# Kernel tuning notes

Measured on AMD Instinct MI355X. Metric: run time of the kernel, lower is better.

## Reference

```python
import jax, jax.numpy as jnp
import numpy as np

VX, VY = 0.2, 0.2
X_OFF = VX / 2 + 0.0          # vx/2 + pc_range[0]
Y_OFF = VY / 2 + (-40.0)      # vy/2 + pc_range[1]
K = 8                          # hardcoded in GCNLayer
BN_EPS = 1e-3
LRELU_SLOPE = 0.2
V, T, C_IN, C_OUT = 4096, 100, 4, 64


def _gcn_layer(x, conv_w, bn_gamma, bn_beta, bn_mean, bn_var):
    """DGCNN EdgeConv layer. x: [N, T, C]. Returns [N, T, O]."""
    N, Tn, C = x.shape
    # KNN on negative squared distance (self included in topk, as in torch code)
    xx = jnp.sum(x * x, axis=-1)                       # [N, T]
    inner = jnp.einsum('ntc,nsc->nts', x, x)           # [N, T, T]
    neg_dist = 2.0 * inner - xx[:, :, None] - xx[:, None, :]
    _, idx = jax.lax.top_k(neg_dist, K)                # [N, T, K]
    # gather neighbor features: nbr[n,t,k,c] = x[n, idx[n,t,k], c]
    nbr = x[jnp.arange(N)[:, None, None], idx]         # [N, T, K, C]
    xc = x[:, :, None, :]                              # [N, T, 1, C]
    edge = jnp.concatenate(
        [nbr - xc, jnp.broadcast_to(xc, (N, Tn, K, C))], axis=-1)  # [N,T,K,2C]
    # 1x1 conv (no bias) + eval-mode BatchNorm + LeakyReLU(0.2)
    h = jnp.einsum('ntkc,oc->ntko', edge, conv_w)      # [N, T, K, O]
    scale = bn_gamma / jnp.sqrt(bn_var + BN_EPS)
    h = (h - bn_mean) * scale + bn_beta
    h = jax.nn.leaky_relu(h, LRELU_SLOPE)
    return jnp.max(h, axis=2)                          # max over k -> [N, T, O]


def setup_inputs() -> dict:
    key = jax.random.key(0)
    k1, k2, k3, k4, k5, k6 = jax.random.split(key, 6)
    features = jax.random.normal(k1, (V, T, C_IN), dtype=jnp.float32)
    num_voxels = jnp.maximum(
        jax.random.randint(k2, (V,), 0, T), 1).astype(jnp.int32)
    coors = jax.random.randint(k3, (V, 4), 0, 352).astype(jnp.int32)
    # GCNLayer params: Conv2d(18, 64, 1, bias=False) + BatchNorm2d(64)
    conv_w = jax.random.normal(k4, (C_OUT, 18), dtype=jnp.float32) * 0.1
    bn_gamma = jnp.ones((C_OUT,), jnp.float32)
    bn_beta = jnp.zeros((C_OUT,), jnp.float32)
    bn_mean = jax.random.normal(k5, (C_OUT,), jnp.float32) * 0.1
    bn_var = 1.0 + 0.1 * jax.random.uniform(k6, (C_OUT,), jnp.float32)
    return {"features": features, "conv_w": conv_w, "bn_gamma": bn_gamma,
            "bn_beta": bn_beta, "bn_mean": bn_mean, "bn_var": bn_var,
            "num_voxels": num_voxels, "coors": coors}


def reference(features, conv_w, bn_gamma, bn_beta, bn_mean, bn_var,
              num_voxels, coors):
    nv = num_voxels.astype(features.dtype)
    # decorate: cluster offsets (xyz - mean) and pillar-center offsets (xy)
    points_mean = jnp.sum(features[:, :, :3], axis=1, keepdims=True) / nv[:, None, None]
    f_cluster = features[:, :, :3] - points_mean                      # [V,T,3]
    fx = features[:, :, 0] - (coors[:, 3].astype(features.dtype)[:, None] * VX + X_OFF)
    fy = features[:, :, 1] - (coors[:, 2].astype(features.dtype)[:, None] * VY + Y_OFF)
    f_center = jnp.stack([fx, fy], axis=-1)                           # [V,T,2]
    feat = jnp.concatenate([features, f_cluster, f_center], axis=-1)  # [V,T,9]
    # padding mask: point t valid iff t < num_voxels[v]
    mask = (jnp.arange(T)[None, :] < num_voxels[:, None]).astype(features.dtype)
    feat = feat * mask[:, :, None]
    # single GCN (last) layer; batch_process chunking is a no-op mathematically
    out = _gcn_layer(feat, conv_w, bn_gamma, bn_beta, bn_mean, bn_var)  # [V,T,64]
    out = out * mask[:, :, None]            # (+ zeros prev_features_out)
    out = jnp.max(out, axis=1)              # max over points -> [V, 64]
    return out
```

## Files before the change

### kernel.cpp

```cpp
#include <hip/hip_runtime.h>

#define TPTS 100
#define CO   64
#define KK   8

__device__ __forceinline__ unsigned umin_(unsigned a, unsigned b) { return a < b ? a : b; }
__device__ __forceinline__ unsigned umax_(unsigned a, unsigned b) { return a > b ? a : b; }

__device__ __forceinline__ unsigned med3u(unsigned a, unsigned b, unsigned c) {
    unsigned d;
    asm("v_med3_u32 %0, %1, %2, %3" : "=v"(d) : "v"(a), "v"(b), "v"(c));
    return d;
}

__device__ __forceinline__ unsigned dist_key(const float4 qt, const float4 qs, unsigned s) {
    float dx = qt.x - qs.x, dy = qt.y - qs.y;
    float dz = qt.z - qs.z, dw = qt.w - qs.w;
    float e = __fmaf_rn(dx, dx, __fmaf_rn(dy, dy, __fmaf_rn(dz, dz, dw * dw)));
    return (__float_as_uint(e) & 0xFFFFFF80u) | s;
}

__device__ __forceinline__ void ins8(unsigned val[KK], unsigned key) {
    #pragma unroll
    for (int k = KK - 1; k >= 1; --k)
        val[k] = med3u(val[k - 1], val[k], key);
    val[0] = umin_(val[0], key);
}

__global__ __launch_bounds__(256) void dgcnn_kernel(
    const float* __restrict__ features,
    const float* __restrict__ conv_w,
    const float* __restrict__ bn_gamma,
    const float* __restrict__ bn_beta,
    const float* __restrict__ bn_mean,
    const float* __restrict__ bn_var,
    const int*  __restrict__ num_voxels,
    const int*  __restrict__ coors,
    float* __restrict__ out)
{
    __shared__ float    s_feat[TPTS][12];
    __shared__ float    s_xx[TPTS];
    __shared__ unsigned s_idxp[TPTS][2];
    __shared__ float    s_red[4][CO];
    __shared__ float    s_mean[4];
    __shared__ union {
        float    stage[TPTS][4];
        _Float16 g16[TPTS][CO];
    } s_u;

    const float INF = __builtin_inff();
    const int v   = blockIdx.x;
    const int tid = threadIdx.x;
    const int nv  = num_voxels[v];

    float4 f = make_float4(0.f, 0.f, 0.f, 0.f);
    if (tid < TPTS) {
        f = reinterpret_cast<const float4*>(features)[v * TPTS + tid];
        *reinterpret_cast<float4*>(&s_u.stage[tid][0]) = f;
    }
    __syncthreads();

    if (tid < 96) {
        int ch = tid >> 5, j = tid & 31;
        float p = s_u.stage[j][ch] + s_u.stage[j + 32][ch] + s_u.stage[j + 64][ch];
        if (j < 4) p += s_u.stage[j + 96][ch];
        #pragma unroll
        for (int off = 16; off >= 1; off >>= 1)
            p += __shfl_xor(p, off, 32);
        if (j == 0) s_mean[ch] = p / (float)nv;
    }
    __syncthreads();

    if (tid < TPTS) {
        float mask = (tid < nv) ? 1.0f : 0.0f;
        float c3 = (float)coors[v * 4 + 3];
        float c2 = (float)coors[v * 4 + 2];
        float r0 = f.x * mask, r1 = f.y * mask, r2 = f.z * mask, r3 = f.w * mask;
        float r4 = (f.x - s_mean[0]) * mask;
        float r5 = (f.y - s_mean[1]) * mask;
        float r6 = (f.z - s_mean[2]) * mask;
        float r7 = (f.x - (c3 * 0.2f + 0.1f)) * mask;
        float r8 = (f.y - (c2 * 0.2f - 39.9f)) * mask;
        float xx = r0*r0 + r1*r1 + r2*r2 + r3*r3 + r4*r4
                 + r5*r5 + r6*r6 + r7*r7 + r8*r8;
        float4* rowv = reinterpret_cast<float4*>(&s_feat[tid][0]);
        rowv[0] = make_float4(1.7320508075688772f * r0,
                              1.7320508075688772f * r1,
                              1.4142135623730951f * r2, r3);
        rowv[1] = make_float4(r4, r5, r6, r7);
        rowv[2] = make_float4(r8, 0.f, 0.f, 0.f);
        s_xx[tid] = xx;
    }

    const int o  = tid & 63;
    const int wv = tid >> 6;
    const float sgn = (bn_gamma[o] < 0.f) ? -1.f : 1.f;
    float w1[9], w2[9];
    #pragma unroll
    for (int c = 0; c < 9; ++c) {
        const float ws = (c == 0 || c == 1) ? 0.57735026918962576f
                       : (c == 2) ? 0.70710678118654752f : 1.f;
        float a = conv_w[o * 18 + c];
        float b = conv_w[o * 18 + 9 + c];
        w1[c] = a * sgn * ws;
        w2[c] = (b - a) * sgn * ws;
    }
    __syncthreads();

    const int nd = (nv + 31) >> 5;

    if (wv < nd) {
        const int trow = wv * 32 + (o & 31);
        const int bsd  = o >> 5;
        if (trow < nv) {
            const float4 qt = *reinterpret_cast<const float4*>(&s_feat[trow][0]);
            unsigned val[KK];
            #pragma unroll
            for (int k = 0; k < KK; ++k) val[k] = 0xFFFFFFFFu;
            int mcnt = TPTS - nv; if (mcnt > KK) mcnt = KK;
            int ha = (nv + mcnt + 1) >> 1; if (ha > nv) ha = nv;
            int s        = bsd ? ha : 0;
            const int se = bsd ? nv : ha;
            #pragma unroll 2
            for (; s < se; ++s) {
                const float4 qs = *reinterpret_cast<const float4*>(&s_feat[s][0]);
                ins8(val, dist_key(qt, qs, (unsigned)s));
            }
            if (bsd) {
                unsigned kmb = __float_as_uint(s_xx[trow]) & 0xFFFFFF80u;
                for (int j = 0; j < mcnt; ++j)
                    ins8(val, kmb | (unsigned)(nv + j));
            }
            unsigned other[KK];
            #pragma unroll
            for (int k = 0; k < KK; ++k) other[k] = __shfl_xor(val[k], 32);
            if (!bsd) {
                unsigned m[KK];
                #pragma unroll
                for (int k = 0; k < KK; ++k)
                    m[k] = umin_(val[k], other[KK - 1 - k]) & 127u;
                unsigned p0 = m[0] | (m[1] << 8) | (m[2] << 16) | (m[3] << 24);
                unsigned p1 = m[4] | (m[5] << 8) | (m[6] << 16) | (m[7] << 24);
                *reinterpret_cast<uint2*>(&s_idxp[trow][0]) = make_uint2(p0, p1);
            }
        }
    }

    {
        int r0 = nv + wv, r1 = nv + wv + 4;
        if (r0 < TPTS) s_u.g16[r0][o] = (_Float16)0.f;
        if (r1 < TPTS) s_u.g16[r1][o] = (_Float16)0.f;
    }

    {
        int sR, step;
        if (nd <= 2) { sR = (wv >= nd) ? (wv - nd) : nv; step = 4 - nd; }
        else         { sR = wv;                          step = 4;      }
        for (; sR < nv; sR += step) {
            const float4* row = reinterpret_cast<const float4*>(&s_feat[sR][0]);
            float4 a = row[0], b = row[1];
            float c8 = s_feat[sR][8];
            float g = a.x * w1[0];
            g = __fmaf_rn(a.y, w1[1], g);
            g = __fmaf_rn(a.z, w1[2], g);
            g = __fmaf_rn(a.w, w1[3], g);
            g = __fmaf_rn(b.x, w1[4], g);
            g = __fmaf_rn(b.y, w1[5], g);
            g = __fmaf_rn(b.z, w1[6], g);
            g = __fmaf_rn(b.w, w1[7], g);
            g = __fmaf_rn(c8,  w1[8], g);
            s_u.g16[sR][o] = (_Float16)g;
        }
    }
    __syncthreads();

    float acc = -INF;
    for (int tt = wv; tt < nv; tt += 4) {
        const float4* row = reinterpret_cast<const float4*>(&s_feat[tt][0]);
        float4 a = row[0], b = row[1];
        float c8 = s_feat[tt][8];
        float base = a.x * w2[0];
        base = __fmaf_rn(a.y, w2[1], base);
        base = __fmaf_rn(a.z, w2[2], base);
        base = __fmaf_rn(a.w, w2[3], base);
        base = __fmaf_rn(b.x, w2[4], base);
        base = __fmaf_rn(b.y, w2[5], base);
        base = __fmaf_rn(b.z, w2[6], base);
        base = __fmaf_rn(b.w, w2[7], base);
        base = __fmaf_rn(c8,  w2[8], base);
        uint2 pk = *reinterpret_cast<const uint2*>(&s_idxp[tt][0]);
        int i0 =  pk.x        & 255, i1 = (pk.x >>  8) & 255;
        int i2 = (pk.x >> 16) & 255, i3 = (pk.x >> 24) & 255;
        int i4 =  pk.y        & 255, i5 = (pk.y >>  8) & 255;
        int i6 = (pk.y >> 16) & 255, i7 = (pk.y >> 24) & 255;
        float g0 = (float)s_u.g16[i0][o], g1 = (float)s_u.g16[i1][o];
        float g2 = (float)s_u.g16[i2][o], g3 = (float)s_u.g16[i3][o];
        float g4 = (float)s_u.g16[i4][o], g5 = (float)s_u.g16[i5][o];
        float g6 = (float)s_u.g16[i6][o], g7 = (float)s_u.g16[i7][o];
        float gm = fmaxf(fmaxf(fmaxf(g0, g1), fmaxf(g2, g3)),
                         fmaxf(fmaxf(g4, g5), fmaxf(g6, g7)));
        acc = fmaxf(acc, gm + base);
    }
    s_red[wv][o] = acc;
    __syncthreads();

    if (tid < CO) {
        float m = fmaxf(fmaxf(s_red[0][tid], s_red[1][tid]),
                        fmaxf(s_red[2][tid], s_red[3][tid]));
        float scale = bn_gamma[tid] / sqrtf(bn_var[tid] + 0.001f);
        float bias  = bn_beta[tid] - bn_mean[tid] * scale;
        float h = m * fabsf(scale) + bias;
        float a = (h > 0.f) ? h : 0.2f * h;
        if (nv < TPTS) a = fmaxf(a, 0.f);
        out[v * CO + tid] = a;
    }
}

extern "C" void kernel_launch(void* const* d_in, const int* in_sizes, int n_in,
                              void* d_out, int out_size, void* d_ws, size_t ws_size,
                              hipStream_t stream) {
    const float* features = (const float*)d_in[0];
    const float* conv_w   = (const float*)d_in[1];
    const float* bn_gamma = (const float*)d_in[2];
    const float* bn_beta  = (const float*)d_in[3];
    const float* bn_mean  = (const float*)d_in[4];
    const float* bn_var   = (const float*)d_in[5];
    const int*   num_vox  = (const int*)d_in[6];
    const int*   coor     = (const int*)d_in[7];
    float* outp = (float*)d_out;
    const int V = in_sizes[6];
    dgcnn_kernel<<<V, 256, 0, stream>>>(features, conv_w, bn_gamma, bn_beta,
                                        bn_mean, bn_var, num_vox, coor, outp);
}
```

Baseline: 111.0 us.

## Use eight waves per voxel and split KNN and gather-table work across waves

Doubles the block to 512 threads (8 waves). Waves without a KNN task now build the fp16 first-half conv table in parallel with the KNN waves. The per-point aggregation loop strides over 8 waves, and the 8-neighbour max is done in fp16 before one conversion. This aims to shorten the serial per-voxel critical path, at the cost of more threads per block, which may limit occupancy and raise sync overhead.

Result: faster. 108.3 us (-2.5%).

```diff
diff --git a/kernel.cpp b/kernel.cpp
--- a/kernel.cpp
+++ b/kernel.cpp
@@ -3,9 +3,11 @@
 #define TPTS 100
 #define CO   64
 #define KK   8
+#define NW   8
 
 __device__ __forceinline__ unsigned umin_(unsigned a, unsigned b) { return a < b ? a : b; }
 __device__ __forceinline__ unsigned umax_(unsigned a, unsigned b) { return a > b ? a : b; }
+__device__ __forceinline__ _Float16 hmax_(_Float16 a, _Float16 b) { return a > b ? a : b; }
 
 __device__ __forceinline__ unsigned med3u(unsigned a, unsigned b, unsigned c) {
     unsigned d;
@@ -27,7 +29,7 @@
     val[0] = umin_(val[0], key);
 }
 
-__global__ __launch_bounds__(256) void dgcnn_kernel(
+__global__ __launch_bounds__(512) void dgcnn_kernel(
     const float* __restrict__ features,
     const float* __restrict__ conv_w,
     const float* __restrict__ bn_gamma,
@@ -41,7 +43,7 @@
     __shared__ float    s_feat[TPTS][12];
     __shared__ float    s_xx[TPTS];
     __shared__ unsigned s_idxp[TPTS][2];
-    __shared__ float    s_red[4][CO];
+    __shared__ float    s_red[NW][CO];
     __shared__ float    s_mean[4];
     __shared__ union {
         float    stage[TPTS][4];
@@ -108,6 +110,11 @@
     __syncthreads();
 
     const int nd = (nv + 31) >> 5;
+
+    {
+        int r0 = nv + wv;
+        if (r0 < TPTS) s_u.g16[r0][o] = (_Float16)0.f;
+    }
 
     if (wv < nd) {
         const int trow = wv * 32 + (o & 31);
@@ -144,19 +151,9 @@
                 *reinterpret_cast<uint2*>(&s_idxp[trow][0]) = make_uint2(p0, p1);
             }
         }
-    }
-
-    {
-        int r0 = nv + wv, r1 = nv + wv + 4;
-        if (r0 < TPTS) s_u.g16[r0][o] = (_Float16)0.f;
-        if (r1 < TPTS) s_u.g16[r1][o] = (_Float16)0.f;
-    }
-
-    {
-        int sR, step;
-        if (nd <= 2) { sR = (wv >= nd) ? (wv - nd) : nv; step = 4 - nd; }
-        else         { sR = wv;                          step = 4;      }
-        for (; sR < nv; sR += step) {
+    } else {
+        const int step = NW - nd;
+        for (int sR = wv - nd; sR < nv; sR += step) {
             const float4* row = reinterpret_cast<const float4*>(&s_feat[sR][0]);
             float4 a = row[0], b = row[1];
             float c8 = s_feat[sR][8];
@@ -175,7 +172,7 @@
     __syncthreads();
 
     float acc = -INF;
-    for (int tt = wv; tt < nv; tt += 4) {
+    for (int tt = wv; tt < nv; tt += NW) {
         const float4* row = reinterpret_cast<const float4*>(&s_feat[tt][0]);
         float4 a = row[0], b = row[1];
         float c8 = s_feat[tt][8];
@@ -193,20 +190,21 @@
         int i2 = (pk.x >> 16) & 255, i3 = (pk.x >> 24) & 255;
         int i4 =  pk.y        & 255, i5 = (pk.y >>  8) & 255;
         int i6 = (pk.y >> 16) & 255, i7 = (pk.y >> 24) & 255;
-        float g0 = (float)s_u.g16[i0][o], g1 = (float)s_u.g16[i1][o];
-        float g2 = (float)s_u.g16[i2][o], g3 = (float)s_u.g16[i3][o];
-        float g4 = (float)s_u.g16[i4][o], g5 = (float)s_u.g16[i5][o];
-        float g6 = (float)s_u.g16[i6][o], g7 = (float)s_u.g16[i7][o];
-        float gm = fmaxf(fmaxf(fmaxf(g0, g1), fmaxf(g2, g3)),
-                         fmaxf(fmaxf(g4, g5), fmaxf(g6, g7)));
-        acc = fmaxf(acc, gm + base);
+        _Float16 g0 = s_u.g16[i0][o], g1 = s_u.g16[i1][o];
+        _Float16 g2 = s_u.g16[i2][o], g3 = s_u.g16[i3][o];
+        _Float16 g4 = s_u.g16[i4][o], g5 = s_u.g16[i5][o];
+        _Float16 g6 = s_u.g16[i6][o], g7 = s_u.g16[i7][o];
+        _Float16 gm = hmax_(hmax_(hmax_(g0, g1), hmax_(g2, g3)),
+                            hmax_(hmax_(g4, g5), hmax_(g6, g7)));
+        acc = fmaxf(acc, (float)gm + base);
     }
     s_red[wv][o] = acc;
     __syncthreads();
 
     if (tid < CO) {
-        float m = fmaxf(fmaxf(s_red[0][tid], s_red[1][tid]),
-                        fmaxf(s_red[2][tid], s_red[3][tid]));
+        float m = s_red[0][tid];
+        #pragma unroll
+        for (int i = 1; i < NW; ++i) m = fmaxf(m, s_red[i][tid]);
         float scale = bn_gamma[tid] / sqrtf(bn_var[tid] + 0.001f);
         float bias  = bn_beta[tid] - bn_mean[tid] * scale;
         float h = m * fabsf(scale) + bias;
@@ -229,6 +227,6 @@
     const int*   coor     = (const int*)d_in[7];
     float* outp = (float*)d_out;
     const int V = in_sizes[6];
-    dgcnn_kernel<<<V, 256, 0, stream>>>(features, conv_w, bn_gamma, bn_beta,
+    dgcnn_kernel<<<V, 512, 0, stream>>>(features, conv_w, bn_gamma, bn_beta,
                                         bn_mean, bn_var, num_vox, coor, outp);
 }
```
